# Performance work log

Measured on AMD Instinct MI355X. Metric: run time of the kernel, lower is better.

The kernel has to match this reference:

```python
import jax, jax.numpy as jnp
import numpy as np

EPS = 1e-5
NC = 183  # num_classes
FUSION_LEVEL = 1

def conv2d(x, w, b=None, pad=0):
    y = jax.lax.conv_general_dilated(x, w, (1, 1), [(pad, pad), (pad, pad)],
                                     dimension_numbers=('NCHW', 'OIHW', 'NCHW'))
    return y if b is None else y + b[None, :, None, None]

def bn(x, g, b, m, v):
    s = g / jnp.sqrt(v + EPS)
    return x * s[None, :, None, None] + (b - m * s)[None, :, None, None]

def deform_conv(x, offset, weight):
    # DCNv1: x [B,C,H,W], offset [B,18,H,W] as (dy,dx) per kernel point, weight [O,C,3,3]
    B, C, H, W = x.shape
    K = 9
    off = offset.reshape(B, K, 2, H, W)
    ky = (jnp.arange(K) // 3 - 1).astype(x.dtype)
    kx = (jnp.arange(K) % 3 - 1).astype(x.dtype)
    yy = jnp.arange(H, dtype=x.dtype)[None, None, :, None] + ky[None, :, None, None] + off[:, :, 0]
    xx = jnp.arange(W, dtype=x.dtype)[None, None, None, :] + kx[None, :, None, None] + off[:, :, 1]
    y0 = jnp.floor(yy)
    x0 = jnp.floor(xx)
    wy = yy - y0
    wx = xx - x0
    def gather(yi, xi):
        valid = ((yi >= 0) & (yi <= H - 1) & (xi >= 0) & (xi <= W - 1))
        yc = jnp.clip(yi, 0, H - 1).astype(jnp.int32)
        xc = jnp.clip(xi, 0, W - 1).astype(jnp.int32)
        g = jax.vmap(lambda im, a, b: im[:, a, b])(x, yc, xc)  # [B,C,K,H,W]
        return g * valid.astype(x.dtype)[:, None]
    s = (gather(y0, x0) * ((1 - wy) * (1 - wx))[:, None]
         + gather(y0, x0 + 1) * ((1 - wy) * wx)[:, None]
         + gather(y0 + 1, x0) * (wy * (1 - wx))[:, None]
         + gather(y0 + 1, x0 + 1) * (wy * wx)[:, None])
    return jnp.einsum('bckhw,ock->bohw', s, weight.reshape(weight.shape[0], C, K))

def resize_bilinear(x, oh, ow):
    # F.interpolate(mode='bilinear', align_corners=True)
    B, C, H, W = x.shape
    if (H, W) == (oh, ow):
        return x
    ys = jnp.linspace(0.0, H - 1.0, oh)
    xs = jnp.linspace(0.0, W - 1.0, ow)
    y0 = jnp.clip(jnp.floor(ys).astype(jnp.int32), 0, H - 2)
    x0 = jnp.clip(jnp.floor(xs).astype(jnp.int32), 0, W - 2)
    wy = (ys - y0).astype(x.dtype)
    wx = (xs - x0).astype(x.dtype)
    r = x[:, :, y0, :] * (1 - wy)[None, None, :, None] + x[:, :, y0 + 1, :] * wy[None, None, :, None]
    return r[:, :, :, x0] * (1 - wx) + r[:, :, :, x0 + 1] * wx

def setup_inputs() -> dict:
    key = jax.random.key(0)
    ks = iter(jax.random.split(key, 64))
    nk = lambda: next(ks)
    B, C = 1, 256
    sizes = [256, 128, 64, 32, 16]
    w = lambda shape, sc: jax.random.normal(nk(), shape, jnp.float32) * sc
    inp = {}
    for i, s in enumerate(sizes):
        inp['feat%d' % i] = jax.random.normal(nk(), (B, C, s, s), jnp.float32)
    inp['off1_w'] = w((18, C, 3, 3), 0.01); inp['off1_b'] = w((18,), 0.01)
    inp['dc1_w'] = w((C, C, 3, 3), 0.02)
    inp['off2_w'] = w((18, C, 3, 3), 0.01); inp['off2_b'] = w((18,), 0.01)
    inp['dc2_w'] = w((C, C, 3, 3), 0.02)
    inp['bn2_g'] = 1.0 + w((C,), 0.01); inp['bn2_b'] = w((C,), 0.01)
    inp['bn2_m'] = w((C,), 0.01); inp['bn2_v'] = jax.random.uniform(nk(), (C,), jnp.float32) + 0.5
    inp['convs_w'] = w((4, C, C, 3, 3), 0.02)
    inp['convs_g'] = 1.0 + w((4, C), 0.01); inp['convs_b'] = w((4, C), 0.01)
    inp['convs_m'] = w((4, C), 0.01); inp['convs_v'] = jax.random.uniform(nk(), (4, C), jnp.float32) + 0.5
    inp['emb_w'] = w((C, C, 1, 1), 0.05)
    inp['emb_g'] = 1.0 + w((C,), 0.01); inp['emb_b'] = w((C,), 0.01)
    inp['emb_m'] = w((C,), 0.01); inp['emb_v'] = jax.random.uniform(nk(), (C,), jnp.float32) + 0.5
    inp['logit_w'] = w((NC, C, 1, 1), 0.05); inp['logit_b'] = w((NC,), 0.01)
    return inp

def reference(feat0, feat1, feat2, feat3, feat4,
              off1_w, off1_b, dc1_w, off2_w, off2_b, dc2_w,
              bn2_g, bn2_b, bn2_m, bn2_v,
              convs_w, convs_g, convs_b, convs_m, convs_v,
              emb_w, emb_g, emb_b, emb_m, emb_v,
              logit_w, logit_b):
    feats = [feat0, feat1, feat2, feat3, feat4]
    def branch(f):
        o = conv2d(f, off1_w, off1_b, pad=1)
        h = deform_conv(f, o, dc1_w)
        o = conv2d(h, off2_w, off2_b, pad=1)
        h = deform_conv(h, o, dc2_w)
        return jax.nn.relu(bn(h, bn2_g, bn2_b, bn2_m, bn2_v))
    x = branch(feats[FUSION_LEVEL])
    H, W = x.shape[-2:]
    for i, f in enumerate(feats):
        if i != FUSION_LEVEL:
            x = x + branch(resize_bilinear(f, H, W))
    for i in range(4):
        x = jax.nn.relu(bn(conv2d(x, convs_w[i], pad=1),
                           convs_g[i], convs_b[i], convs_m[i], convs_v[i]))
    mask_pred = conv2d(x, logit_w, logit_b, pad=0)
    emb = jax.nn.relu(bn(conv2d(x, emb_w, pad=0), emb_g, emb_b, emb_m, emb_v))
    return (mask_pred, emb)
```

## Files before the change

kernel.cpp:

```cpp
#include <hip/hip_runtime.h>
#include <hip/hip_bf16.h>
#include <stdint.h>

#define EPS_BN 1e-5f
constexpr int PP = 16384;
using short8 = __attribute__((ext_vector_type(8))) short;
using f32x4  = __attribute__((ext_vector_type(4))) float;
typedef unsigned short u16;

__device__ inline float bf2f(u16 u) {
  unsigned v = ((unsigned)u) << 16; float f; __builtin_memcpy(&f, &v, 4); return f;
}
__device__ inline u16 f2bf(float f) {
  unsigned b; __builtin_memcpy(&b, &f, 4);
  b += 0x7FFFu + ((b >> 16) & 1u);
  return (u16)(b >> 16);
}

#define GLD16(g, l) __builtin_amdgcn_global_load_lds( \
    (__attribute__((address_space(1))) void*)(void*)(g), \
    (__attribute__((address_space(3))) void*)(void*)(l), 16, 0, 0)

__global__ void bn_prep_k(const float* __restrict__ g0, const float* __restrict__ b0,
                          const float* __restrict__ m0, const float* __restrict__ v0,
                          const float* __restrict__ cg, const float* __restrict__ cb,
                          const float* __restrict__ cm, const float* __restrict__ cv,
                          const float* __restrict__ eg, const float* __restrict__ eb,
                          const float* __restrict__ em, const float* __restrict__ ev,
                          float* __restrict__ scale, float* __restrict__ shift) {
  int c = threadIdx.x;
  float s = g0[c] * rsqrtf(v0[c] + EPS_BN);
  scale[c] = s; shift[c] = b0[c] - m0[c] * s;
#pragma unroll
  for (int i = 0; i < 4; ++i) {
    float si = cg[i*256+c] * rsqrtf(cv[i*256+c] + EPS_BN);
    scale[(1+i)*256+c] = si; shift[(1+i)*256+c] = cb[i*256+c] - cm[i*256+c]*si;
  }
  float se = eg[c] * rsqrtf(ev[c] + EPS_BN);
  scale[5*256+c] = se; shift[5*256+c] = eb[c] - em[c]*se;
}

__global__ void prep_w_k(const float* __restrict__ w, u16* __restrict__ W2,
                         int Ocnt, int KK, int NPAD) {
  int idx = blockIdx.x * 256 + threadIdx.x;
  int total = NPAD * KK * 256;
  if (idx >= total) return;
  int o = idx / (KK * 256); int rem = idx - o * (KK * 256);
  int kpt = rem >> 8, c = rem & 255;
  W2[idx] = (o < Ocnt) ? f2bf(w[(o * 256 + c) * KK + kpt]) : (u16)0;
}

__global__ void tr_k(const float* __restrict__ in, u16* __restrict__ out, int P) {
  __shared__ float tile[64][65];
  int p0 = blockIdx.x * 64, c0 = blockIdx.y * 64;
  int t = threadIdx.x;
  int tl = t & 63, tg = t >> 6;
#pragma unroll
  for (int i = 0; i < 16; ++i) {
    int c = tg * 16 + i;
    tile[c][tl] = in[(size_t)(c0 + c) * P + p0 + tl];
  }
  __syncthreads();
  int px = t >> 2, cq = t & 3;
#pragma unroll
  for (int pass = 0; pass < 2; ++pass) {
    int c = cq * 8 + pass * 32;
    u16 r[8];
#pragma unroll
    for (int j = 0; j < 8; ++j) r[j] = f2bf(tile[c + j][px]);
    *(short8*)(out + (size_t)(p0 + px) * 256 + c0 + c) = *(short8*)r;
  }
}

__global__ void rs_k(const u16* __restrict__ in, u16* __restrict__ out, int Hs) {
  int t = threadIdx.x;
  int p = blockIdx.x * 8 + (t >> 5), q = t & 31;
  int oy = p >> 7, ox = p & 127;
  float sc = (float)(Hs - 1) / 127.0f;
  float ys = oy * sc, xs = ox * sc;
  int y0 = (int)ys; if (y0 > Hs - 2) y0 = Hs - 2;
  int x0 = (int)xs; if (x0 > Hs - 2) x0 = Hs - 2;
  float wy = ys - (float)y0, wx = xs - (float)x0;
  const u16* b00 = in + ((size_t)(y0 * Hs + x0)) * 256 + q * 8;
  short8 v00 = *(const short8*)b00;
  short8 v01 = *(const short8*)(b00 + 256);
  short8 v10 = *(const short8*)(b00 + (size_t)Hs * 256);
  short8 v11 = *(const short8*)(b00 + (size_t)Hs * 256 + 256);
  u16 r[8];
#pragma unroll
  for (int j = 0; j < 8; ++j) {
    float a = bf2f((u16)v00[j]) * (1.f - wx) + bf2f((u16)v01[j]) * wx;
    float b = bf2f((u16)v10[j]) * (1.f - wx) + bf2f((u16)v11[j]) * wx;
    r[j] = f2bf(a * (1.f - wy) + b * wy);
  }
  *(short8*)(out + (size_t)p * 256 + q * 8) = *(short8*)r;
}

template<int EPI>
__launch_bounds__(256, 3)
__global__ void dc_k(const u16* __restrict__ A, const u16* __restrict__ Bw,
                     const float* __restrict__ offs, u16* __restrict__ oB,
                     const float* __restrict__ scale, const float* __restrict__ shift) {
  __shared__ u16 sB[2][256 * 32];
  const int t = threadIdx.x, w = t >> 6, l = t & 63, lr = l & 15, lq = l >> 4;
  int bx = blockIdx.x; { int n8 = gridDim.x >> 3; bx = (bx & 7) * n8 + (bx >> 3); }
  const int p0 = bx * 64;
  const int gp = p0 + w * 16 + lr;
  const int pl = gp & 16383, lb = gp & ~16383;

  f32x4 acc[16];
#pragma unroll
  for (int n = 0; n < 16; ++n) acc[n] = (f32x4){0.f, 0.f, 0.f, 0.f};

  float wgt[4];
  int   cb[4];
  short8 cv[4];
  float2 onext;
  const short8 z8 = (short8){0, 0, 0, 0, 0, 0, 0, 0};

  unsigned boff[4];
#pragma unroll
  for (int it = 0; it < 4; ++it) {
    int ch = it * 256 + t, row = ch >> 2, s = ch & 3;
    int cl = s ^ ((row ^ (row >> 2)) & 3);
    boff[it] = (unsigned)(row * 2304 + cl * 8);
  }

  onext = *(const float2*)(offs + (size_t)gp * 32);

  auto newKpt = [&](int kpt) {
    float2 o2 = onext;
    if (kpt < 8) onext = *(const float2*)(offs + (size_t)gp * 32 + 2 * (kpt + 1));
    float yy = (float)((pl >> 7) + kpt / 3 - 1) + o2.x;
    float xx = (float)((pl & 127) + kpt % 3 - 1) + o2.y;
    float yf = floorf(yy), xf = floorf(xx);
    float fy = yy - yf, fx = xx - xf;
    int y0 = (int)yf, x0 = (int)xf;
    bool va = (unsigned)y0 < 128u, vb = (unsigned)(y0 + 1) < 128u;
    bool ha = (unsigned)x0 < 128u, hb = (unsigned)(x0 + 1) < 128u;
    wgt[0] = (1.f - fy) * (1.f - fx); cb[0] = (va && ha) ? lb + (y0 << 7) + x0 : -1;
    wgt[1] = (1.f - fy) * fx;         cb[1] = (va && hb) ? lb + (y0 << 7) + x0 + 1 : -1;
    wgt[2] = fy * (1.f - fx);         cb[2] = (vb && ha) ? lb + ((y0 + 1) << 7) + x0 : -1;
    wgt[3] = fy * fx;                 cb[3] = (vb && hb) ? lb + ((y0 + 1) << 7) + x0 + 1 : -1;
  };
  auto loadC = [&](int ks) {
    int cc = ((ks & 7) << 5) + lq * 8;
#pragma unroll
    for (int c = 0; c < 4; ++c)
      cv[c] = (cb[c] >= 0) ? *(const short8*)(A + (size_t)cb[c] * 256 + cc) : z8;
  };

  newKpt(0);
  loadC(0);
  const int laneoff = lr * 64 + ((lq ^ ((lr ^ (lr >> 2)) & 3)) << 4);

  for (int ks = 0; ks < 72; ++ks) {
    {
      const u16* bbase = Bw + ks * 32;
      char* dst = (char*)sB[ks & 1] + w * 1024;
#pragma unroll
      for (int it = 0; it < 4; ++it) GLD16(bbase + boff[it], dst + it * 4096);
    }
    short8 af;
    {
      u16 rr[8];
      const unsigned* u0 = (const unsigned*)&cv[0];
      const unsigned* u1 = (const unsigned*)&cv[1];
      const unsigned* u2 = (const unsigned*)&cv[2];
      const unsigned* u3 = (const unsigned*)&cv[3];
#pragma unroll
      for (int j2 = 0; j2 < 4; ++j2) {
        float lo, hi;
        {
          unsigned a0 = u0[j2], a1 = u1[j2], a2 = u2[j2], a3 = u3[j2];
          float l0, h0, l1, h1, l2, h2, l3, h3;
          unsigned tl_, th_;
          tl_ = a0 << 16; th_ = a0 & 0xFFFF0000u;
          __builtin_memcpy(&l0, &tl_, 4); __builtin_memcpy(&h0, &th_, 4);
          tl_ = a1 << 16; th_ = a1 & 0xFFFF0000u;
          __builtin_memcpy(&l1, &tl_, 4); __builtin_memcpy(&h1, &th_, 4);
          tl_ = a2 << 16; th_ = a2 & 0xFFFF0000u;
          __builtin_memcpy(&l2, &tl_, 4); __builtin_memcpy(&h2, &th_, 4);
          tl_ = a3 << 16; th_ = a3 & 0xFFFF0000u;
          __builtin_memcpy(&l3, &tl_, 4); __builtin_memcpy(&h3, &th_, 4);
          lo = wgt[0] * l0 + wgt[1] * l1 + wgt[2] * l2 + wgt[3] * l3;
          hi = wgt[0] * h0 + wgt[1] * h1 + wgt[2] * h2 + wgt[3] * h3;
        }
        __hip_bfloat16 hl = __float2bfloat16(lo);
        __hip_bfloat16 hh = __float2bfloat16(hi);
        rr[2 * j2]     = *(u16*)&hl;
        rr[2 * j2 + 1] = *(u16*)&hh;
      }
      af = *(short8*)rr;
    }
    if (ks < 71 && (((ks + 1) & 7) == 0)) newKpt((ks + 1) >> 3);
    __syncthreads();
    if (ks < 71) loadC(ks + 1);
    const char* base = (const char*)sB[ks & 1] + laneoff;
    __builtin_amdgcn_s_setprio(1);
#pragma unroll
    for (int n = 0; n < 16; ++n) {
      short8 bfr = *(const short8*)(base + n * 1024);
      acc[n] = __builtin_amdgcn_mfma_f32_16x16x32_bf16(af, bfr, acc[n], 0, 0, 0);
    }
    __builtin_amdgcn_s_setprio(0);
  }

  {
    int prow = p0 + w * 16 + lq * 4;
#pragma unroll
    for (int n = 0; n < 16; ++n) {
      int oc = n * 16 + lr;
      float sc = 1.f, sh = 0.f;
      if constexpr (EPI == 3) { sc = scale[oc]; sh = shift[oc]; }
#pragma unroll
      for (int q = 0; q < 4; ++q) {
        float v = acc[n][q];
        if constexpr (EPI == 3) v = fmaxf(v * sc + sh, 0.f);
        oB[(size_t)(prow + q) * 256 + oc] = f2bf(v);
      }
    }
  }
}

template<int MODE, int AM, int AN, int MW, int NW, int EPI>
__launch_bounds__(MW*NW*64)
__global__ void mm_k(const u16* __restrict__ A, const u16* __restrict__ B,
                     const u16* __restrict__ zbuf,
                     float* __restrict__ oF, u16* __restrict__ oB,
                     const float* __restrict__ bias,
                     const float* __restrict__ scale, const float* __restrict__ shift,
                     int Ktot, int ksteps, int OutN) {
  constexpr int BM = MW * AM * 16, BN = NW * AN * 16, NT = MW * NW * 64;
  constexpr int AITS = BM * 8 / NT, BITS = BN * 8 / NT;
  __shared__ u16 sA[BM * 64];
  __shared__ u16 sB[BN * 64];
  char* sAb = (char*)sA; char* sBb = (char*)sB;
  const int t = threadIdx.x;
  const int w = t >> 6, l = t & 63;
  const int lr = l & 15, lq = l >> 4;
  const int wm = w / NW, wn = w % NW;
  int bx = blockIdx.x;
  { int n8 = gridDim.x >> 3; bx = (bx & 7) * n8 + (bx >> 3); }
  const int p0 = bx * BM, n0 = blockIdx.y * BN;

  f32x4 acc[AM][AN];
#pragma unroll
  for (int m = 0; m < AM; ++m)
#pragma unroll
    for (int n = 0; n < AN; ++n) acc[m][n] = (f32x4){0.f, 0.f, 0.f, 0.f};

  for (int ks = 0; ks < ksteps; ++ks) {
    int k0 = ks * 64;
#pragma unroll
    for (int it = 0; it < BITS; ++it) {
      int ch = it * NT + t;
      int row = ch >> 3, cl = (ch & 7) ^ (row & 7);
      GLD16(B + (size_t)(n0 + row) * Ktot + k0 + cl * 8, sBb + it * (NT * 16) + w * 1024);
    }
    if constexpr (MODE == 0) {
#pragma unroll
      for (int it = 0; it < AITS; ++it) {
        int ch = it * NT + t;
        int row = ch >> 3, cl = (ch & 7) ^ (row & 7);
        GLD16(A + (size_t)(p0 + row) * Ktot + k0 + cl * 8, sAb + it * (NT * 16) + w * 1024);
      }
    } else {
      int kpt = k0 >> 8, c0 = k0 & 255;
      int dy = kpt / 3 - 1, dx = kpt % 3 - 1;
#pragma unroll
      for (int it = 0; it < AITS; ++it) {
        int ch = it * NT + t;
        int row = ch >> 3, cl = (ch & 7) ^ (row & 7);
        int gp = p0 + row; int lvl = gp >> 14, pl = gp & 16383;
        int yy = (pl >> 7) + dy, xx = (pl & 127) + dx;
        const u16* src = ((unsigned)yy < 128u && (unsigned)xx < 128u)
            ? A + ((size_t)(lvl << 14) + (yy << 7) + xx) * 256 + c0 + cl * 8
            : zbuf;
        GLD16(src, sAb + it * (NT * 16) + w * 1024);
      }
    }
    __syncthreads();
    short8 af[AM], bfr[AN];
#pragma unroll
    for (int h = 0; h < 2; ++h) {
#pragma unroll
      for (int m = 0; m < AM; ++m) {
        int ar = wm * AM * 16 + m * 16 + lr;
        af[m] = *(const short8*)(sAb + ar * 128 + (((h * 4 + lq) ^ (ar & 7)) << 4));
      }
#pragma unroll
      for (int n = 0; n < AN; ++n) {
        int br = wn * AN * 16 + n * 16 + lr;
        bfr[n] = *(const short8*)(sBb + br * 128 + (((h * 4 + lq) ^ (br & 7)) << 4));
      }
#pragma unroll
      for (int m = 0; m < AM; ++m)
#pragma unroll
        for (int n = 0; n < AN; ++n)
          acc[m][n] = __builtin_amdgcn_mfma_f32_16x16x32_bf16(af[m], bfr[n], acc[m][n], 0, 0, 0);
    }
    __syncthreads();
  }

#pragma unroll
  for (int m = 0; m < AM; ++m) {
    int prow = p0 + wm * AM * 16 + m * 16 + lq * 4;
#pragma unroll
    for (int n = 0; n < AN; ++n) {
      int oc = n0 + wn * AN * 16 + n * 16 + lr;
      if constexpr (EPI == 1) {
        float bs = (oc < 18) ? bias[oc] : 0.f;
#pragma unroll
        for (int r = 0; r < 4; ++r) oF[(size_t)(prow + r) * 32 + oc] = acc[m][n][r] + bs;
      } else if constexpr (EPI == 2) {
#pragma unroll
        for (int r = 0; r < 4; ++r) oB[(size_t)(prow + r) * 256 + oc] = f2bf(acc[m][n][r]);
      } else if constexpr (EPI == 3) {
        float sc = scale[oc], sh = shift[oc];
#pragma unroll
        for (int r = 0; r < 4; ++r)
          oB[(size_t)(prow + r) * 256 + oc] = f2bf(fmaxf(acc[m][n][r] * sc + sh, 0.f));
      } else if constexpr (EPI == 4) {
        if (oc < OutN) {
          float bs = bias[oc];
          float4 v = {acc[m][n][0] + bs, acc[m][n][1] + bs, acc[m][n][2] + bs, acc[m][n][3] + bs};
          *(float4*)(oF + (size_t)oc * PP + prow) = v;
        }
      } else {
        float sc = scale[oc], sh = shift[oc];
        float4 v = {fmaxf(acc[m][n][0] * sc + sh, 0.f), fmaxf(acc[m][n][1] * sc + sh, 0.f),
                    fmaxf(acc[m][n][2] * sc + sh, 0.f), fmaxf(acc[m][n][3] * sc + sh, 0.f)};
        *(float4*)(oF + (size_t)oc * PP + prow) = v;
      }
    }
  }
}

__global__ void sum5_k(const u16* __restrict__ H2, u16* __restrict__ out) {
  size_t base = ((size_t)blockIdx.x * 256 + threadIdx.x) * 8;
  float a[8] = {0,0,0,0,0,0,0,0};
#pragma unroll
  for (int lvl = 0; lvl < 5; ++lvl) {
    short8 v = *(const short8*)(H2 + (size_t)lvl * PP * 256 + base);
#pragma unroll
    for (int j = 0; j < 8; ++j) a[j] += bf2f((u16)v[j]);
  }
  u16 r[8];
#pragma unroll
  for (int j = 0; j < 8; ++j) r[j] = f2bf(a[j]);
  *(short8*)(out + base) = *(short8*)r;
}

extern "C" void kernel_launch(void* const* d_in, const int* in_sizes, int n_in,
                              void* d_out, int out_size, void* d_ws, size_t ws_size,
                              hipStream_t stream) {
  const float* feats[5];
  for (int i = 0; i < 5; ++i) feats[i] = (const float*)d_in[i];
  int fsz[5] = {256, 128, 64, 32, 16};
  const float* off1_w = (const float*)d_in[5];
  const float* off1_b = (const float*)d_in[6];
  const float* dc1_w  = (const float*)d_in[7];
  const float* off2_w = (const float*)d_in[8];
  const float* off2_b = (const float*)d_in[9];
  const float* dc2_w  = (const float*)d_in[10];
  const float* bn2_g  = (const float*)d_in[11];
  const float* bn2_b  = (const float*)d_in[12];
  const float* bn2_m  = (const float*)d_in[13];
  const float* bn2_v  = (const float*)d_in[14];
  const float* convs_w = (const float*)d_in[15];
  const float* convs_g = (const float*)d_in[16];
  const float* convs_b = (const float*)d_in[17];
  const float* convs_m = (const float*)d_in[18];
  const float* convs_v = (const float*)d_in[19];
  const float* emb_w  = (const float*)d_in[20];
  const float* emb_g  = (const float*)d_in[21];
  const float* emb_b  = (const float*)d_in[22];
  const float* emb_m  = (const float*)d_in[23];
  const float* emb_v  = (const float*)d_in[24];
  const float* logit_w = (const float*)d_in[25];
  const float* logit_b = (const float*)d_in[26];

  char* ws = (char*)d_ws;
  size_t off = 0;
  auto alloc = [&](size_t bytes) { char* p = ws + off; off += (bytes + 255) & ~255ull; return p; };
  float* bnscale = (float*)alloc(6 * 256 * 4);
  float* bnshift = (float*)alloc(6 * 256 * 4);
  u16* zbuf = (u16*)alloc(256);
  u16* W2_off1 = (u16*)alloc((size_t)32 * 2304 * 2);
  u16* W2_off2 = (u16*)alloc((size_t)32 * 2304 * 2);
  u16* W2_dc1  = (u16*)alloc((size_t)256 * 2304 * 2);
  u16* W2_dc2  = (u16*)alloc((size_t)256 * 2304 * 2);
  u16* W2_c    = (u16*)alloc((size_t)4 * 256 * 2304 * 2);
  u16* W2_logit = (u16*)alloc((size_t)256 * 256 * 2);
  u16* W2_emb   = (u16*)alloc((size_t)256 * 256 * 2);
  u16* R_all  = (u16*)alloc((size_t)5 * PP * 256 * 2);
  u16* H_all  = (u16*)alloc((size_t)5 * PP * 256 * 2);
  u16* H2_all = (u16*)alloc((size_t)5 * PP * 256 * 2);
  float* O    = (float*)alloc((size_t)5 * PP * 32 * 4);
  u16* Xb     = (u16*)alloc((size_t)PP * 256 * 2);
  u16* Ftmp = H_all;
  u16* cb0 = R_all;
  u16* cb1 = R_all + (size_t)PP * 256;

  hipMemsetAsync(zbuf, 0, 256, stream);
  bn_prep_k<<<1, 256, 0, stream>>>(bn2_g, bn2_b, bn2_m, bn2_v, convs_g, convs_b, convs_m, convs_v,
                                   emb_g, emb_b, emb_m, emb_v, bnscale, bnshift);
  auto pw = [&](const float* src, u16* dst, int Ocnt, int KK, int NPAD) {
    int total = NPAD * KK * 256;
    prep_w_k<<<(total + 255) / 256, 256, 0, stream>>>(src, dst, Ocnt, KK, NPAD);
  };
  pw(off1_w, W2_off1, 18, 9, 32);
  pw(off2_w, W2_off2, 18, 9, 32);
  pw(dc1_w,  W2_dc1, 256, 9, 256);
  pw(dc2_w,  W2_dc2, 256, 9, 256);
  for (int i = 0; i < 4; ++i) pw(convs_w + (size_t)i * 2304 * 256, W2_c + (size_t)i * 2304 * 256, 256, 9, 256);
  pw(logit_w, W2_logit, 183, 1, 256);
  pw(emb_w,   W2_emb,   256, 1, 256);

  const dim3 blk(256);
  for (int lvl = 0; lvl < 5; ++lvl) {
    int P = fsz[lvl] * fsz[lvl];
    u16* dst = (lvl == 1) ? (R_all + (size_t)PP * 256) : Ftmp;
    tr_k<<<dim3(P / 64, 4), blk, 0, stream>>>(feats[lvl], dst, P);
    if (lvl != 1)
      rs_k<<<dim3(PP / 8), blk, 0, stream>>>(Ftmp, R_all + (size_t)lvl * PP * 256, fsz[lvl]);
  }

  constexpr int MG = 5 * PP;
  mm_k<1, 2, 2, 4, 1, 1><<<dim3(MG / 128, 1), blk, 0, stream>>>(
      R_all, W2_off1, zbuf, O, nullptr, off1_b, nullptr, nullptr, 2304, 36, 32);
  dc_k<2><<<dim3(MG / 64), blk, 0, stream>>>(R_all, W2_dc1, O, H_all, nullptr, nullptr);
  mm_k<1, 2, 2, 4, 1, 1><<<dim3(MG / 128, 1), blk, 0, stream>>>(
      H_all, W2_off2, zbuf, O, nullptr, off2_b, nullptr, nullptr, 2304, 36, 32);
  dc_k<3><<<dim3(MG / 64), blk, 0, stream>>>(H_all, W2_dc2, O, H2_all, bnscale, bnshift);

  sum5_k<<<dim3(2048), blk, 0, stream>>>(H2_all, Xb);

  const u16* cur = Xb;
  u16* cbuf[2] = {cb0, cb1};
  for (int i = 0; i < 4; ++i) {
    mm_k<1, 2, 4, 2, 2, 3><<<dim3(PP / 64, 2), blk, 0, stream>>>(
        cur, W2_c + (size_t)i * 2304 * 256, zbuf, nullptr, cbuf[i & 1],
        nullptr, bnscale + (1 + i) * 256, bnshift + (1 + i) * 256, 2304, 36, 256);
    cur = cbuf[i & 1];
  }

  float* outp = (float*)d_out;
  mm_k<0, 2, 4, 2, 2, 4><<<dim3(PP / 64, 2), blk, 0, stream>>>(
      cur, W2_logit, zbuf, outp, nullptr, logit_b, nullptr, nullptr, 256, 4, 183);
  mm_k<0, 2, 4, 2, 2, 5><<<dim3(PP / 64, 2), blk, 0, stream>>>(
      cur, W2_emb, zbuf, outp + (size_t)183 * PP, nullptr, nullptr,
      bnscale + 5 * 256, bnshift + 5 * 256, 256, 4, 256);
}
```

Measured before the change: 879.3 us.

## Triple-buffer pre-swizzled deform-conv weights and split conv tiles finer

New measurement: 825.8 us. 6.1% less time.

```diff
diff --git a/kernel.cpp b/kernel.cpp
--- a/kernel.cpp
+++ b/kernel.cpp
@@ -16,6 +16,7 @@
   b += 0x7FFFu + ((b >> 16) & 1u);
   return (u16)(b >> 16);
 }
+__device__ inline float u2f(unsigned x) { float f; __builtin_memcpy(&f, &x, 4); return f; }
 
 #define GLD16(g, l) __builtin_amdgcn_global_load_lds( \
     (__attribute__((address_space(1))) void*)(void*)(g), \
@@ -48,6 +49,16 @@
   int o = idx / (KK * 256); int rem = idx - o * (KK * 256);
   int kpt = rem >> 8, c = rem & 255;
   W2[idx] = (o < Ocnt) ? f2bf(w[(o * 256 + c) * KK + kpt]) : (u16)0;
+}
+
+__global__ void prep_wf_k(const float* __restrict__ w, u16* __restrict__ W2f) {
+  int idx = blockIdx.x * 256 + threadIdx.x;
+  int ks = idx >> 13, r = idx & 8191;
+  int n = r >> 9, r2 = r & 511;
+  int lane = r2 >> 3, j = r2 & 7;
+  int k = ks * 32 + ((lane >> 4) << 3) + j;
+  int oc = n * 16 + (lane & 15);
+  W2f[idx] = f2bf(w[(oc * 256 + (k & 255)) * 9 + (k >> 8)]);
 }
 
 __global__ void tr_k(const float* __restrict__ in, u16* __restrict__ out, int P) {
@@ -98,10 +109,10 @@
 
 template<int EPI>
 __launch_bounds__(256, 3)
-__global__ void dc_k(const u16* __restrict__ A, const u16* __restrict__ Bw,
+__global__ void dc_k(const u16* __restrict__ A, const u16* __restrict__ Bw2,
                      const float* __restrict__ offs, u16* __restrict__ oB,
                      const float* __restrict__ scale, const float* __restrict__ shift) {
-  __shared__ u16 sB[2][256 * 32];
+  __shared__ u16 sB[3][256 * 32];
   const int t = threadIdx.x, w = t >> 6, l = t & 63, lr = l & 15, lq = l >> 4;
   int bx = blockIdx.x; { int n8 = gridDim.x >> 3; bx = (bx & 7) * n8 + (bx >> 3); }
   const int p0 = bx * 64;
@@ -117,14 +128,6 @@
   short8 cv[4];
   float2 onext;
   const short8 z8 = (short8){0, 0, 0, 0, 0, 0, 0, 0};
-
-  unsigned boff[4];
-#pragma unroll
-  for (int it = 0; it < 4; ++it) {
-    int ch = it * 256 + t, row = ch >> 2, s = ch & 3;
-    int cl = s ^ ((row ^ (row >> 2)) & 3);
-    boff[it] = (unsigned)(row * 2304 + cl * 8);
-  }
 
   onext = *(const float2*)(offs + (size_t)gp * 32);
 
@@ -149,18 +152,19 @@
     for (int c = 0; c < 4; ++c)
       cv[c] = (cb[c] >= 0) ? *(const short8*)(A + (size_t)cb[c] * 256 + cc) : z8;
   };
-
+  auto stageB = [&](int ks) {
+    const u16* src = Bw2 + (size_t)ks * 8192 + t * 8;
+    char* dst = (char*)sB[ks % 3] + t * 16;
+#pragma unroll
+    for (int it = 0; it < 4; ++it) GLD16(src + it * 2048, dst + it * 4096);
+  };
+
+  stageB(0);
   newKpt(0);
   loadC(0);
-  const int laneoff = lr * 64 + ((lq ^ ((lr ^ (lr >> 2)) & 3)) << 4);
 
   for (int ks = 0; ks < 72; ++ks) {
-    {
-      const u16* bbase = Bw + ks * 32;
-      char* dst = (char*)sB[ks & 1] + w * 1024;
-#pragma unroll
-      for (int it = 0; it < 4; ++it) GLD16(bbase + boff[it], dst + it * 4096);
-    }
+    if (ks < 71) stageB(ks + 1);
     short8 af;
     {
       u16 rr[8];
@@ -170,22 +174,11 @@
       const unsigned* u3 = (const unsigned*)&cv[3];
 #pragma unroll
       for (int j2 = 0; j2 < 4; ++j2) {
-        float lo, hi;
-        {
-          unsigned a0 = u0[j2], a1 = u1[j2], a2 = u2[j2], a3 = u3[j2];
-          float l0, h0, l1, h1, l2, h2, l3, h3;
-          unsigned tl_, th_;
-          tl_ = a0 << 16; th_ = a0 & 0xFFFF0000u;
-          __builtin_memcpy(&l0, &tl_, 4); __builtin_memcpy(&h0, &th_, 4);
-          tl_ = a1 << 16; th_ = a1 & 0xFFFF0000u;
-          __builtin_memcpy(&l1, &tl_, 4); __builtin_memcpy(&h1, &th_, 4);
-          tl_ = a2 << 16; th_ = a2 & 0xFFFF0000u;
-          __builtin_memcpy(&l2, &tl_, 4); __builtin_memcpy(&h2, &th_, 4);
-          tl_ = a3 << 16; th_ = a3 & 0xFFFF0000u;
-          __builtin_memcpy(&l3, &tl_, 4); __builtin_memcpy(&h3, &th_, 4);
-          lo = wgt[0] * l0 + wgt[1] * l1 + wgt[2] * l2 + wgt[3] * l3;
-          hi = wgt[0] * h0 + wgt[1] * h1 + wgt[2] * h2 + wgt[3] * h3;
-        }
+        unsigned a0 = u0[j2], a1 = u1[j2], a2 = u2[j2], a3 = u3[j2];
+        float lo = wgt[0] * u2f(a0 << 16) + wgt[1] * u2f(a1 << 16)
+                 + wgt[2] * u2f(a2 << 16) + wgt[3] * u2f(a3 << 16);
+        float hi = wgt[0] * u2f(a0 & 0xFFFF0000u) + wgt[1] * u2f(a1 & 0xFFFF0000u)
+                 + wgt[2] * u2f(a2 & 0xFFFF0000u) + wgt[3] * u2f(a3 & 0xFFFF0000u);
         __hip_bfloat16 hl = __float2bfloat16(lo);
         __hip_bfloat16 hh = __float2bfloat16(hi);
         rr[2 * j2]     = *(u16*)&hl;
@@ -194,9 +187,11 @@
       af = *(short8*)rr;
     }
     if (ks < 71 && (((ks + 1) & 7) == 0)) newKpt((ks + 1) >> 3);
-    __syncthreads();
+    __builtin_amdgcn_sched_barrier(0);
+    __builtin_amdgcn_s_barrier();
+    __builtin_amdgcn_sched_barrier(0);
     if (ks < 71) loadC(ks + 1);
-    const char* base = (const char*)sB[ks & 1] + laneoff;
+    const char* base = (const char*)sB[ks % 3] + l * 16;
     __builtin_amdgcn_s_setprio(1);
 #pragma unroll
     for (int n = 0; n < 16; ++n) {
@@ -412,8 +407,8 @@
   };
   pw(off1_w, W2_off1, 18, 9, 32);
   pw(off2_w, W2_off2, 18, 9, 32);
-  pw(dc1_w,  W2_dc1, 256, 9, 256);
-  pw(dc2_w,  W2_dc2, 256, 9, 256);
+  prep_wf_k<<<2304, 256, 0, stream>>>(dc1_w, W2_dc1);
+  prep_wf_k<<<2304, 256, 0, stream>>>(dc2_w, W2_dc2);
   for (int i = 0; i < 4; ++i) pw(convs_w + (size_t)i * 2304 * 256, W2_c + (size_t)i * 2304 * 256, 256, 9, 256);
   pw(logit_w, W2_logit, 183, 1, 256);
   pw(emb_w,   W2_emb,   256, 1, 256);
@@ -440,7 +435,7 @@
   const u16* cur = Xb;
   u16* cbuf[2] = {cb0, cb1};
   for (int i = 0; i < 4; ++i) {
-    mm_k<1, 2, 4, 2, 2, 3><<<dim3(PP / 64, 2), blk, 0, stream>>>(
+    mm_k<1, 2, 2, 2, 2, 3><<<dim3(PP / 64, 4), blk, 0, stream>>>(
         cur, W2_c + (size_t)i * 2304 * 256, zbuf, nullptr, cbuf[i & 1],
         nullptr, bnscale + (1 + i) * 256, bnshift + (1 + i) * 256, 2304, 36, 256);
     cur = cbuf[i & 1];
```
